# Kernel optimization log

Measured on AMD Instinct MI355X. Metric: run time of the kernel, lower is better.

The kernel has to match this reference:

```python
import jax, jax.numpy as jnp
import numpy as np
from jax import lax

B, T, D, H, K = 8, 1024, 1024, 16, 3
DK = D // H


def setup_inputs() -> dict:
    key = jax.random.key(0)
    ks = jax.random.split(key, 12)
    s = 0.02
    queries = jax.random.normal(ks[0], (B, T, D), dtype=jnp.float32)
    keys = jax.random.normal(ks[1], (B, T, D), dtype=jnp.float32)
    values = jax.random.normal(ks[2], (B, T, D), dtype=jnp.float32)
    # causal mask: True = masked (strict upper triangle)
    attn_mask = jnp.triu(jnp.ones((T, T), dtype=bool), k=1)
    # key padding mask: last 128 keys padded for every batch element
    src_key_padding_mask = jnp.broadcast_to(jnp.arange(T) >= T - 128, (B, T))
    conv_q_w = jax.random.normal(ks[3], (D, D, K), dtype=jnp.float32) * s  # (out, in, k)
    conv_q_b = jax.random.normal(ks[4], (D,), dtype=jnp.float32) * s
    conv_k_w = jax.random.normal(ks[5], (D, D, K), dtype=jnp.float32) * s
    conv_k_b = jax.random.normal(ks[6], (D,), dtype=jnp.float32) * s
    v_w = jax.random.normal(ks[7], (D, D), dtype=jnp.float32) * s   # torch Linear weight [out,in]
    v_b = jax.random.normal(ks[8], (D,), dtype=jnp.float32) * s
    out_w = jax.random.normal(ks[9], (D, D), dtype=jnp.float32) * s
    out_b = jax.random.normal(ks[10], (D,), dtype=jnp.float32) * s
    return {"queries": queries, "keys": keys, "values": values,
            "attn_mask": attn_mask, "src_key_padding_mask": src_key_padding_mask,
            "conv_q_w": conv_q_w, "conv_q_b": conv_q_b,
            "conv_k_w": conv_k_w, "conv_k_b": conv_k_b,
            "v_w": v_w, "v_b": v_b, "out_w": out_w, "out_b": out_b}


def _conv1d_same(x, w, b):
    # x: [B, T, D] -> conv over time with 'same' padding (pad_l=(K-1)//2, pad_r=K//2)
    pad_l, pad_r = (K - 1) // 2, K // 2
    xc = jnp.pad(x.transpose(0, 2, 1), ((0, 0), (0, 0), (pad_l, pad_r)))  # [B, D, T+K-1]
    y = lax.conv_general_dilated(xc, w, window_strides=(1,), padding='VALID',
                                 dimension_numbers=('NCH', 'OIH', 'NCH'))  # [B, D, T]
    return y.transpose(0, 2, 1) + b  # [B, T, D]


def _attention(queries, keys, values, attn_mask, key_padding_mask,
               conv_q_w, conv_q_b, conv_k_w, conv_k_b, v_w, v_b, out_w, out_b):
    q_out = _conv1d_same(queries, conv_q_w, conv_q_b)  # [B, Tq, D]
    k_out = _conv1d_same(keys, conv_k_w, conv_k_b)     # [B, Tk, D]
    v_out = values @ v_w.T + v_b                        # [B, Tk, D]

    Q = q_out.reshape(B, T, H, DK).transpose(0, 2, 1, 3)  # [B, H, Tq, dk]
    Kh = k_out.reshape(B, T, H, DK).transpose(0, 2, 1, 3)
    V = v_out.reshape(B, T, H, DK).transpose(0, 2, 1, 3)

    scores = jnp.einsum('bhqd,bhkd->bhqk', Q, Kh) / jnp.sqrt(jnp.float32(DK))
    neg = jnp.float32(-jnp.inf)
    scores = jnp.where(key_padding_mask[:, None, None, :], neg, scores)
    scores = jnp.where(attn_mask[None, None, :, :], neg, scores)
    attn_weights = jax.nn.softmax(scores, axis=-1)  # dropout is identity at eval
    attn_output = jnp.einsum('bhqk,bhkd->bhqd', attn_weights, V)
    attn_output = attn_output.transpose(0, 2, 1, 3).reshape(B, T, D)
    return attn_output @ out_w.T + out_b, attn_weights


def reference(queries, keys, values, attn_mask, src_key_padding_mask,
              conv_q_w, conv_q_b, conv_k_w, conv_k_b, v_w, v_b, out_w, out_b):
    return _attention(queries, keys, values, attn_mask, src_key_padding_mask,
                      conv_q_w, conv_q_b, conv_k_w, conv_k_b, v_w, v_b, out_w, out_b)
```

## Files before the change

### kernel.cpp

```cpp
#include <hip/hip_runtime.h>

typedef unsigned short u16;
typedef unsigned int   u32;
typedef __bf16 bf16x8 __attribute__((ext_vector_type(8)));
typedef float  f32x4  __attribute__((ext_vector_type(4)));
typedef const __attribute__((address_space(1))) u32* gas1_t;
typedef __attribute__((address_space(3))) u32*       las3_t;

#define DEV static __device__ __forceinline__
#define MFMA16(a, b, c) __builtin_amdgcn_mfma_f32_16x16x32_bf16((a), (b), (c), 0, 0, 0)

DEV u16 f2b(float f) {
  u32 u = __builtin_bit_cast(u32, f);
  return (u16)((u + 0x7fffu + ((u >> 16) & 1u)) >> 16);
}
DEV float b2f(u16 h) { return __builtin_bit_cast(float, (u32)h << 16); }

DEV void stage16(const void* g, void* l) {
  __builtin_amdgcn_global_load_lds((gas1_t)g, (las3_t)l, 16, 0, 0);
}

DEV int rfl(int x) { return __builtin_amdgcn_readfirstlane(x); }

extern "C" __global__ __launch_bounds__(256)
void k_prep(const float* __restrict__ s0, const float* __restrict__ s1,
            const float* __restrict__ s2, const float* __restrict__ s3,
            const float* __restrict__ s4, const float* __restrict__ wq,
            const float* __restrict__ wk, u16* __restrict__ dqkv,
            u16* __restrict__ dvw, u16* __restrict__ dow,
            u16* __restrict__ wtbase, u16* __restrict__ zbuf) {
  __shared__ float ls[3072];
  const int y = blockIdx.y, tid = threadIdx.x;
  if (y < 5) {
    const float* src = y == 0 ? s0 : y == 1 ? s1 : y == 2 ? s2 : y == 3 ? s3 : s4;
    u16* dst = y < 3 ? dqkv + (size_t)y * 8388608 : (y == 3 ? dvw : dow);
    const int n4 = y < 3 ? 2097152 : 262144;
    int i = blockIdx.x * 256 + tid;
    int st = gridDim.x * 256;
    for (; i < n4; i += st) {
      float4 v = ((const float4*)src)[i];
      ushort4 o;
      o.x = f2b(v.x); o.y = f2b(v.y); o.z = f2b(v.z); o.w = f2b(v.w);
      ((ushort4*)dst)[i] = o;
    }
  } else if (y < 7) {
    const int o = blockIdx.x, zz = y - 5;
    const float* src = (zz ? wk : wq) + (size_t)o * 3072;
#pragma unroll
    for (int s = 0; s < 3; ++s)
      ((float4*)ls)[s * 256 + tid] = ((const float4*)src)[s * 256 + tid];
    __syncthreads();
    u16* dst = wtbase + (size_t)zz * 3145728 + (size_t)o * 3072;
#pragma unroll
    for (int s = 0; s < 12; ++s) {
      int j = s * 256 + tid;
      int k = j >> 10, ii = j & 1023;
      dst[j] = f2b(ls[ii * 3 + k]);
    }
  } else {
    if (blockIdx.x == 0) zbuf[tid] = 0;
  }
}

template <int FUSED3, int OUTF32>
__global__ __launch_bounds__(256)
void k_gemm(const u16* __restrict__ Abase, const u16* __restrict__ Btbase,
            const float* __restrict__ b0, const float* __restrict__ b1,
            const float* __restrict__ b2, void* __restrict__ Cbase,
            u16* __restrict__ vT, const u16* __restrict__ zbuf) {
  __shared__ __align__(16) u16 smem[17408];
  const int z = FUSED3 ? blockIdx.z : 0;
  const bool conv = FUSED3 && (z < 2);
  const int K = conv ? 3072 : 1024;
  const u16* A = Abase + (size_t)z * 8388608;
  const u16* Bt = Btbase + (size_t)z * 3145728;
  const float* bias = z == 0 ? b0 : z == 1 ? b1 : b2;
  const int tid = threadIdx.x, lane = tid & 63, wave = tid >> 6;
  const int wm = wave >> 1, wn = wave & 1;
  const int l15 = lane & 15, gr = lane >> 4;
  const int r0 = blockIdx.y * 128, n0 = blockIdx.x * 128;
  const int srow = tid >> 3, scol = (tid & 7) * 8;
  u16* sA = smem;
  f32x4 acc[4][4] = {};

  if (conv) {
    u16* sB = smem + 8320;
    const int bb = r0 >> 10;
    const int tb = (r0 & 1023) - 1;
#pragma unroll 1
    for (int t = 0; t < 16; ++t) {
      const int c0 = t * 64;
#pragma unroll
      for (int s = 0; s < 5; ++s) {
        const int e = s * 256 + tid;
        if (e < 1040) {
          const int lr = e >> 3, ch = (e & 7) * 8;
          const int tt = tb + lr;
          const u16* g = ((u32)tt < 1024u)
              ? (A + (((size_t)((bb << 10) + tt)) << 10) + c0 + ch)
              : (zbuf + ch);
          stage16(g, (char*)smem + rfl((s * 256 + wave * 64) * 16));
        }
      }
#pragma unroll
      for (int s3 = 0; s3 < 3; ++s3) {
#pragma unroll
        for (int s = 0; s < 4; ++s) {
          const int row = s * 32 + srow;
          stage16(Bt + (size_t)(n0 + row) * 3072 + s3 * 1024 + c0 + scol,
                  (char*)smem + rfl(16640 + (s * 256 + wave * 64) * 16));
        }
        __syncthreads();
#pragma unroll
        for (int ks = 0; ks < 2; ++ks) {
          bf16x8 af[4], bfr[4];
          const int koff = ks * 32 + gr * 8;
#pragma unroll
          for (int f = 0; f < 4; ++f)
            af[f] = *(const bf16x8*)&sA[(wm * 64 + f * 16 + l15 + s3) * 64 + koff];
#pragma unroll
          for (int f = 0; f < 4; ++f)
            bfr[f] = *(const bf16x8*)&sB[(wn * 64 + f * 16 + l15) * 64 + koff];
#pragma unroll
          for (int i = 0; i < 4; ++i)
#pragma unroll
            for (int j = 0; j < 4; ++j)
              acc[i][j] = MFMA16(af[i], bfr[j], acc[i][j]);
        }
        __syncthreads();
      }
    }
  } else {
    u16* sB = smem + 8192;
    const int nt = K >> 6;
    for (int t = 0; t < nt; ++t) {
      const int k0 = t * 64;
#pragma unroll
      for (int s = 0; s < 4; ++s) {
        const int row = s * 32 + srow;
        stage16(A + (size_t)(r0 + row) * K + k0 + scol,
                (char*)smem + rfl((s * 256 + wave * 64) * 16));
        stage16(Bt + (size_t)(n0 + row) * K + k0 + scol,
                (char*)smem + rfl(16384 + (s * 256 + wave * 64) * 16));
      }
      __syncthreads();
#pragma unroll
      for (int ks = 0; ks < 2; ++ks) {
        bf16x8 af[4], bfr[4];
        const int koff = ks * 32 + gr * 8;
#pragma unroll
        for (int f = 0; f < 4; ++f)
          af[f] = *(const bf16x8*)&sA[(wm * 64 + f * 16 + l15) * 64 + koff];
#pragma unroll
        for (int f = 0; f < 4; ++f)
          bfr[f] = *(const bf16x8*)&sB[(wn * 64 + f * 16 + l15) * 64 + koff];
#pragma unroll
        for (int i = 0; i < 4; ++i)
#pragma unroll
          for (int j = 0; j < 4; ++j)
            acc[i][j] = MFMA16(af[i], bfr[j], acc[i][j]);
      }
      __syncthreads();
    }
  }

  if (FUSED3 && z == 2) {
    u16* tp = smem;
#pragma unroll
    for (int i = 0; i < 4; ++i)
#pragma unroll
      for (int j = 0; j < 4; ++j) {
        const int cl = wn * 64 + j * 16 + l15;
        const float bv = bias[n0 + cl];
        const int rl0 = wm * 64 + i * 16 + gr * 4;
        union { u16 h[4]; ushort4 v4; } tv;
#pragma unroll
        for (int r = 0; r < 4; ++r) tv.h[r] = f2b(acc[i][j][r] + bv);
        *(ushort4*)&tp[cl * 136 + rl0] = tv.v4;
      }
    __syncthreads();
    const int bb2 = r0 >> 10, tof = r0 & 1023;
    const int drb = tid >> 4, ch16 = (tid & 15) * 8;
#pragma unroll
    for (int g = 0; g < 8; ++g) {
      const int dr = g * 16 + drb;
      uint4 v4 = *(const uint4*)&tp[dr * 136 + ch16];
      *(uint4*)&vT[(((size_t)((bb2 << 10) + n0 + dr)) << 10) + tof + ch16] = v4;
    }
  } else {
    void* Cout = OUTF32 ? Cbase : (void*)((u16*)Cbase + (size_t)z * 8388608);
#pragma unroll
    for (int i = 0; i < 4; ++i)
#pragma unroll
      for (int j = 0; j < 4; ++j) {
        const int colg = n0 + wn * 64 + j * 16 + l15;
        const float bv = bias[colg];
#pragma unroll
        for (int r = 0; r < 4; ++r) {
          const int rowg = r0 + wm * 64 + i * 16 + gr * 4 + r;
          float v = acc[i][j][r] + bv;
          if (OUTF32) ((float*)Cout)[(size_t)rowg * 1024 + colg] = v;
          else        ((u16*)Cout)[(size_t)rowg * 1024 + colg] = f2b(v);
        }
      }
  }
}

__global__ __launch_bounds__(256)
void k_attn(const u16* __restrict__ Qg, const u16* __restrict__ Kg,
            const u16* __restrict__ Vtg, float* __restrict__ Wout,
            u16* __restrict__ Og) {
  __shared__ __align__(16) u16 sK[64 * 64];
  __shared__ __align__(16) u16 sV[64 * 64];
  __shared__ __align__(16) u16 sP[4][32 * 64];
  const int tid = threadIdx.x, lane = tid & 63, wave = tid >> 6;
  const int l15 = lane & 15, gr = lane >> 4;
  const int q0 = blockIdx.x * 128, h = blockIdx.y, b = blockIdx.z;
  const u16* Qh = Qg + ((size_t)b << 20) + h * 64;
  const u16* Kh = Kg + ((size_t)b << 20) + h * 64;
  const u16* Vh = Vtg + ((size_t)b << 20) + ((size_t)(h * 64) << 10);
  float* Wh = Wout + ((size_t)(b * 16 + h) << 20);
  const int qw0 = q0 + wave * 32;
  const int rmaxw = (qw0 + 31 < 895) ? (qw0 + 31) : 895;
  const int ktw = (rmaxw >> 6) + 1;
  const int rmaxg = (q0 + 127 < 895) ? (q0 + 127) : 895;
  const int ktmax = (rmaxg >> 6) + 1;

  bf16x8 qf[2][2];
#pragma unroll
  for (int i = 0; i < 2; ++i)
#pragma unroll
    for (int ks = 0; ks < 2; ++ks)
      qf[i][ks] = *(const bf16x8*)
          &Qh[(size_t)(qw0 + i * 16 + l15) * 1024 + ks * 32 + gr * 8];

  float l[2][4] = {};

  for (int kt = 0; kt < ktmax; ++kt) {
#pragma unroll
    for (int s = 0; s < 2; ++s) {
      int e = s * 256 + tid;
      int row = e >> 3, col = (e & 7) * 8;
      stage16(Kh + (size_t)(kt * 64 + row) * 1024 + col,
              (char*)sK + rfl((s * 256 + wave * 64) * 16));
    }
    __syncthreads();
    if (kt < ktw) {
      f32x4 sc[2][4] = {};
#pragma unroll
      for (int ks = 0; ks < 2; ++ks) {
        bf16x8 bfr[4];
        const int koff = ks * 32 + gr * 8;
#pragma unroll
        for (int f = 0; f < 4; ++f)
          bfr[f] = *(const bf16x8*)&sK[(f * 16 + l15) * 64 + koff];
#pragma unroll
        for (int i = 0; i < 2; ++i)
#pragma unroll
          for (int f = 0; f < 4; ++f) sc[i][f] = MFMA16(qf[i][ks], bfr[f], sc[i][f]);
      }
#pragma unroll
      for (int i = 0; i < 2; ++i)
#pragma unroll
        for (int r = 0; r < 4; ++r) {
          const int rowg = qw0 + i * 16 + gr * 4 + r;
          float ss = 0.f;
#pragma unroll
          for (int f = 0; f < 4; ++f) {
            const int colg = kt * 64 + f * 16 + l15;
            if (colg <= rowg && colg < 896) ss += __expf(sc[i][f][r] * 0.125f);
          }
#pragma unroll
          for (int d = 1; d < 16; d <<= 1) ss += __shfl_xor(ss, d, 16);
          l[i][r] += ss;
        }
    }
    __syncthreads();
  }

  float rl[2][4];
#pragma unroll
  for (int i = 0; i < 2; ++i)
#pragma unroll
    for (int r = 0; r < 4; ++r) rl[i][r] = 1.f / l[i][r];

  for (int r = 0; r < 32; ++r) {
    float* wrow = Wh + (size_t)(qw0 + r) * 1024;
    for (int c = ktw * 64 + lane * 4; c < 1024; c += 256)
      *(float4*)&wrow[c] = make_float4(0.f, 0.f, 0.f, 0.f);
  }

  f32x4 oa[2][4] = {};
  for (int kt = 0; kt < ktmax; ++kt) {
#pragma unroll
    for (int s = 0; s < 2; ++s) {
      int e = s * 256 + tid;
      int row = e >> 3, col = (e & 7) * 8;
      stage16(Kh + (size_t)(kt * 64 + row) * 1024 + col,
              (char*)sK + rfl((s * 256 + wave * 64) * 16));
      stage16(Vh + (size_t)row * 1024 + kt * 64 + col,
              (char*)sV + rfl((s * 256 + wave * 64) * 16));
    }
    __syncthreads();
    if (kt < ktw) {
      f32x4 sc[2][4] = {};
#pragma unroll
      for (int ks = 0; ks < 2; ++ks) {
        bf16x8 bfr[4];
        const int koff = ks * 32 + gr * 8;
#pragma unroll
        for (int f = 0; f < 4; ++f)
          bfr[f] = *(const bf16x8*)&sK[(f * 16 + l15) * 64 + koff];
#pragma unroll
        for (int i = 0; i < 2; ++i)
#pragma unroll
          for (int f = 0; f < 4; ++f) sc[i][f] = MFMA16(qf[i][ks], bfr[f], sc[i][f]);
      }
#pragma unroll
      for (int i = 0; i < 2; ++i)
#pragma unroll
        for (int r = 0; r < 4; ++r) {
          const int rowl = i * 16 + gr * 4 + r;
          const int rowg = qw0 + rowl;
#pragma unroll
          for (int f = 0; f < 4; ++f) {
            const int colt = f * 16 + l15;
            const int colg = kt * 64 + colt;
            float p = (colg <= rowg && colg < 896)
                          ? __expf(sc[i][f][r] * 0.125f) * rl[i][r] : 0.f;
            sP[wave][rowl * 64 + colt] = f2b(p);
          }
        }
      asm volatile("s_waitcnt lgkmcnt(0)" ::: "memory");
#pragma unroll
      for (int ks = 0; ks < 2; ++ks) {
        bf16x8 paf[2], vf[4];
        const int koff = ks * 32 + gr * 8;
        paf[0] = *(const bf16x8*)&sP[wave][l15 * 64 + koff];
        paf[1] = *(const bf16x8*)&sP[wave][(16 + l15) * 64 + koff];
#pragma unroll
        for (int f = 0; f < 4; ++f)
          vf[f] = *(const bf16x8*)&sV[(f * 16 + l15) * 64 + koff];
#pragma unroll
        for (int i = 0; i < 2; ++i)
#pragma unroll
          for (int f = 0; f < 4; ++f) oa[i][f] = MFMA16(paf[i], vf[f], oa[i][f]);
      }
#pragma unroll
      for (int rr = 0; rr < 8; ++rr) {
        const int rowl = rr * 4 + gr;
        const int c4 = l15 * 4;
        union { u16 h[4]; uint2 v2; } t;
        t.v2 = *(const uint2*)&sP[wave][rowl * 64 + c4];
        float4 o;
        o.x = b2f(t.h[0]); o.y = b2f(t.h[1]); o.z = b2f(t.h[2]); o.w = b2f(t.h[3]);
        *(float4*)&Wh[(size_t)(qw0 + rowl) * 1024 + kt * 64 + c4] = o;
      }
    }
    __syncthreads();
  }
#pragma unroll
  for (int i = 0; i < 2; ++i)
#pragma unroll
    for (int f = 0; f < 4; ++f)
#pragma unroll
      for (int r = 0; r < 4; ++r) {
        const int rowg = qw0 + i * 16 + gr * 4 + r;
        const int dd = f * 16 + l15;
        Og[((size_t)b * 1024 + rowg) * 1024 + h * 64 + dd] = f2b(oa[i][f][r]);
      }
}

extern "C" void kernel_launch(void* const* d_in, const int* in_sizes, int n_in,
                              void* d_out, int out_size, void* d_ws, size_t ws_size,
                              hipStream_t stream) {
  const float* queries  = (const float*)d_in[0];
  const float* keys     = (const float*)d_in[1];
  const float* values   = (const float*)d_in[2];
  const float* conv_q_w = (const float*)d_in[5];
  const float* conv_q_b = (const float*)d_in[6];
  const float* conv_k_w = (const float*)d_in[7];
  const float* conv_k_b = (const float*)d_in[8];
  const float* v_w      = (const float*)d_in[9];
  const float* v_b      = (const float*)d_in[10];
  const float* out_w    = (const float*)d_in[11];
  const float* out_b    = (const float*)d_in[12];

  float* out0 = (float*)d_out;
  float* outW = out0 + (size_t)8 * 1024 * 1024;

  char* W = (char*)d_ws;
  u16* qkv_bf = (u16*)(W + (size_t)0);
  u16* wt     = (u16*)(W + (size_t)50331648);
  u16* ow_t   = (u16*)(W + (size_t)65011712);
  u16* q_out  = (u16*)(W + (size_t)67108864);
  u16* zbuf   = (u16*)(W + (size_t)117440512);
  u16* vw_t   = wt + (size_t)2 * 3145728;
  u16* k_out  = q_out + (size_t)8388608;
  u16* v_outT = q_out + (size_t)2 * 8388608;
  u16* a_out  = qkv_bf + 8388608;

  dim3 blk(256);
  k_prep<<<dim3(1024, 8), blk, 0, stream>>>(queries, keys, values, v_w, out_w,
                                            conv_q_w, conv_k_w, qkv_bf, vw_t,
                                            ow_t, wt, zbuf);

  k_gemm<1, 0><<<dim3(8, 64, 3), blk, 0, stream>>>(
      qkv_bf, wt, conv_q_b, conv_k_b, v_b, (void*)q_out, v_outT, zbuf);
  k_attn<<<dim3(8, 16, 8), blk, 0, stream>>>(q_out, k_out, v_outT, outW, a_out);
  k_gemm<0, 1><<<dim3(8, 64, 1), blk, 0, stream>>>(
      a_out, ow_t, out_b, out_b, out_b, (void*)out0, v_outT, zbuf);
}
```

Before: 445.3 us.

## Split conv GEMMs into dedicated 512-thread kernel with 128x256 tiles

The Q/K convolution GEMMs move out of the fused 3-way k_gemm into a new k_conv512 kernel. It uses 512 threads and 128x256 output tiles, so each staged A tile (with its halo rows) is reused across twice as many output columns. The V projection now runs as a separate k_gemm launch selected by a z offset. This cuts A-tile reloads for the conv path, in exchange for an extra launch, higher LDS use per block, and uncoalesced scalar bf16 stores in the epilogue.

```diff
diff --git a/kernel.cpp b/kernel.cpp
--- a/kernel.cpp
+++ b/kernel.cpp
@@ -62,16 +62,95 @@
   }
 }
 
+extern "C" __global__ __launch_bounds__(512)
+void k_conv512(const u16* __restrict__ Abase, const u16* __restrict__ Btbase,
+               const float* __restrict__ b0, const float* __restrict__ b1,
+               u16* __restrict__ Cbase, const u16* __restrict__ zbuf) {
+  __shared__ __align__(16) u16 smem[24704];
+  const int bid = blockIdx.x;
+  const int xz = bid & 7;
+  const int z = xz >> 2;
+  const int n0 = (xz & 3) * 256;
+  const int r0 = (bid >> 3) * 128;
+  const u16* A = Abase + (size_t)z * 8388608;
+  const u16* Bt = Btbase + (size_t)z * 3145728;
+  const float* bias = z ? b1 : b0;
+  const int tid = threadIdx.x, lane = tid & 63, wave = tid >> 6;
+  const int wm = wave >> 2, wn = wave & 3;
+  const int l15 = lane & 15, gr = lane >> 4;
+  const int srow = tid >> 3, scol = (tid & 7) * 8;
+  u16* sA = smem;
+  u16* sB = smem + 8320;
+  f32x4 acc[4][4] = {};
+  const int bb = r0 >> 10;
+  const int tb = (r0 & 1023) - 1;
+#pragma unroll 1
+  for (int t = 0; t < 16; ++t) {
+    const int c0 = t * 64;
+#pragma unroll
+    for (int s = 0; s < 3; ++s) {
+      const int e = s * 512 + tid;
+      if (e < 1040) {
+        const int lr = e >> 3, ch = (e & 7) * 8;
+        const int tt = tb + lr;
+        const u16* g = ((u32)tt < 1024u)
+            ? (A + (((size_t)((bb << 10) + tt)) << 10) + c0 + ch)
+            : (zbuf + ch);
+        stage16(g, (char*)smem + rfl((s * 512 + wave * 64) * 16));
+      }
+    }
+#pragma unroll
+    for (int s3 = 0; s3 < 3; ++s3) {
+#pragma unroll
+      for (int s = 0; s < 4; ++s) {
+        const int row = s * 64 + srow;
+        stage16(Bt + (size_t)(n0 + row) * 3072 + s3 * 1024 + c0 + scol,
+                (char*)smem + rfl(16640 + (s * 512 + wave * 64) * 16));
+      }
+      __syncthreads();
+#pragma unroll
+      for (int ks = 0; ks < 2; ++ks) {
+        bf16x8 af[4], bfr[4];
+        const int koff = ks * 32 + gr * 8;
+#pragma unroll
+        for (int f = 0; f < 4; ++f)
+          af[f] = *(const bf16x8*)&sA[(wm * 64 + f * 16 + l15 + s3) * 64 + koff];
+#pragma unroll
+        for (int f = 0; f < 4; ++f)
+          bfr[f] = *(const bf16x8*)&sB[(wn * 64 + f * 16 + l15) * 64 + koff];
+#pragma unroll
+        for (int i = 0; i < 4; ++i)
+#pragma unroll
+          for (int j = 0; j < 4; ++j)
+            acc[i][j] = MFMA16(af[i], bfr[j], acc[i][j]);
+      }
+      __syncthreads();
+    }
+  }
+  u16* Cout = Cbase + (size_t)z * 8388608;
+#pragma unroll
+  for (int i = 0; i < 4; ++i)
+#pragma unroll
+    for (int j = 0; j < 4; ++j) {
+      const int colg = n0 + wn * 64 + j * 16 + l15;
+      const float bv = bias[colg];
+#pragma unroll
+      for (int r = 0; r < 4; ++r) {
+        const int rowg = r0 + wm * 64 + i * 16 + gr * 4 + r;
+        Cout[(size_t)rowg * 1024 + colg] = f2b(acc[i][j][r] + bv);
+      }
+    }
+}
+
 template <int FUSED3, int OUTF32>
 __global__ __launch_bounds__(256)
 void k_gemm(const u16* __restrict__ Abase, const u16* __restrict__ Btbase,
             const float* __restrict__ b0, const float* __restrict__ b1,
             const float* __restrict__ b2, void* __restrict__ Cbase,
-            u16* __restrict__ vT, const u16* __restrict__ zbuf) {
+            u16* __restrict__ vT, const u16* __restrict__ zbuf, int zoff) {
   __shared__ __align__(16) u16 smem[17408];
-  const int z = FUSED3 ? blockIdx.z : 0;
-  const bool conv = FUSED3 && (z < 2);
-  const int K = conv ? 3072 : 1024;
+  const int z = FUSED3 ? ((int)blockIdx.z + zoff) : 0;
+  const int K = 1024;
   const u16* A = Abase + (size_t)z * 8388608;
   const u16* Bt = Btbase + (size_t)z * 3145728;
   const float* bias = z == 0 ? b0 : z == 1 ? b1 : b2;
@@ -81,87 +160,38 @@
   const int r0 = blockIdx.y * 128, n0 = blockIdx.x * 128;
   const int srow = tid >> 3, scol = (tid & 7) * 8;
   u16* sA = smem;
+  u16* sB = smem + 8192;
   f32x4 acc[4][4] = {};
 
-  if (conv) {
-    u16* sB = smem + 8320;
-    const int bb = r0 >> 10;
-    const int tb = (r0 & 1023) - 1;
-#pragma unroll 1
-    for (int t = 0; t < 16; ++t) {
-      const int c0 = t * 64;
-#pragma unroll
-      for (int s = 0; s < 5; ++s) {
-        const int e = s * 256 + tid;
-        if (e < 1040) {
-          const int lr = e >> 3, ch = (e & 7) * 8;
-          const int tt = tb + lr;
-          const u16* g = ((u32)tt < 1024u)
-              ? (A + (((size_t)((bb << 10) + tt)) << 10) + c0 + ch)
-              : (zbuf + ch);
-          stage16(g, (char*)smem + rfl((s * 256 + wave * 64) * 16));
-        }
-      }
-#pragma unroll
-      for (int s3 = 0; s3 < 3; ++s3) {
-#pragma unroll
-        for (int s = 0; s < 4; ++s) {
-          const int row = s * 32 + srow;
-          stage16(Bt + (size_t)(n0 + row) * 3072 + s3 * 1024 + c0 + scol,
-                  (char*)smem + rfl(16640 + (s * 256 + wave * 64) * 16));
-        }
-        __syncthreads();
-#pragma unroll
-        for (int ks = 0; ks < 2; ++ks) {
-          bf16x8 af[4], bfr[4];
-          const int koff = ks * 32 + gr * 8;
-#pragma unroll
-          for (int f = 0; f < 4; ++f)
-            af[f] = *(const bf16x8*)&sA[(wm * 64 + f * 16 + l15 + s3) * 64 + koff];
-#pragma unroll
-          for (int f = 0; f < 4; ++f)
-            bfr[f] = *(const bf16x8*)&sB[(wn * 64 + f * 16 + l15) * 64 + koff];
-#pragma unroll
-          for (int i = 0; i < 4; ++i)
-#pragma unroll
-            for (int j = 0; j < 4; ++j)
-              acc[i][j] = MFMA16(af[i], bfr[j], acc[i][j]);
-        }
-        __syncthreads();
-      }
-    }
-  } else {
-    u16* sB = smem + 8192;
-    const int nt = K >> 6;
-    for (int t = 0; t < nt; ++t) {
-      const int k0 = t * 64;
-#pragma unroll
-      for (int s = 0; s < 4; ++s) {
-        const int row = s * 32 + srow;
-        stage16(A + (size_t)(r0 + row) * K + k0 + scol,
-                (char*)smem + rfl((s * 256 + wave * 64) * 16));
-        stage16(Bt + (size_t)(n0 + row) * K + k0 + scol,
-                (char*)smem + rfl(16384 + (s * 256 + wave * 64) * 16));
-      }
-      __syncthreads();
-#pragma unroll
-      for (int ks = 0; ks < 2; ++ks) {
-        bf16x8 af[4], bfr[4];
-        const int koff = ks * 32 + gr * 8;
-#pragma unroll
-        for (int f = 0; f < 4; ++f)
-          af[f] = *(const bf16x8*)&sA[(wm * 64 + f * 16 + l15) * 64 + koff];
-#pragma unroll
-        for (int f = 0; f < 4; ++f)
-          bfr[f] = *(const bf16x8*)&sB[(wn * 64 + f * 16 + l15) * 64 + koff];
-#pragma unroll
-        for (int i = 0; i < 4; ++i)
-#pragma unroll
-          for (int j = 0; j < 4; ++j)
-            acc[i][j] = MFMA16(af[i], bfr[j], acc[i][j]);
-      }
-      __syncthreads();
-    }
+  const int nt = K >> 6;
+  for (int t = 0; t < nt; ++t) {
+    const int k0 = t * 64;
+#pragma unroll
+    for (int s = 0; s < 4; ++s) {
+      const int row = s * 32 + srow;
+      stage16(A + (size_t)(r0 + row) * K + k0 + scol,
+              (char*)smem + rfl((s * 256 + wave * 64) * 16));
+      stage16(Bt + (size_t)(n0 + row) * K + k0 + scol,
+              (char*)smem + rfl(16384 + (s * 256 + wave * 64) * 16));
+    }
+    __syncthreads();
+#pragma unroll
+    for (int ks = 0; ks < 2; ++ks) {
+      bf16x8 af[4], bfr[4];
+      const int koff = ks * 32 + gr * 8;
+#pragma unroll
+      for (int f = 0; f < 4; ++f)
+        af[f] = *(const bf16x8*)&sA[(wm * 64 + f * 16 + l15) * 64 + koff];
+#pragma unroll
+      for (int f = 0; f < 4; ++f)
+        bfr[f] = *(const bf16x8*)&sB[(wn * 64 + f * 16 + l15) * 64 + koff];
+#pragma unroll
+      for (int i = 0; i < 4; ++i)
+#pragma unroll
+        for (int j = 0; j < 4; ++j)
+          acc[i][j] = MFMA16(af[i], bfr[j], acc[i][j]);
+    }
+    __syncthreads();
   }
 
   if (FUSED3 && z == 2) {
@@ -331,7 +361,7 @@
             sP[wave][rowl * 64 + colt] = f2b(p);
           }
         }
-      asm volatile("s_waitcnt lgkmcnt(0)" ::: "memory");
+    asm volatile("s_waitcnt lgkmcnt(0)" ::: "memory");
 #pragma unroll
       for (int ks = 0; ks < 2; ++ks) {
         bf16x8 paf[2], vf[4];
@@ -405,9 +435,11 @@
                                             conv_q_w, conv_k_w, qkv_bf, vw_t,
                                             ow_t, wt, zbuf);
 
-  k_gemm<1, 0><<<dim3(8, 64, 3), blk, 0, stream>>>(
-      qkv_bf, wt, conv_q_b, conv_k_b, v_b, (void*)q_out, v_outT, zbuf);
+  k_conv512<<<dim3(512), dim3(512), 0, stream>>>(
+      qkv_bf, wt, conv_q_b, conv_k_b, q_out, zbuf);
+  k_gemm<1, 0><<<dim3(8, 64, 1), blk, 0, stream>>>(
+      qkv_bf, wt, conv_q_b, conv_k_b, v_b, (void*)q_out, v_outT, zbuf, 2);
   k_attn<<<dim3(8, 16, 8), blk, 0, stream>>>(q_out, k_out, v_outT, outW, a_out);
   k_gemm<0, 1><<<dim3(8, 64, 1), blk, 0, stream>>>(
-      a_out, ow_t, out_b, out_b, out_b, (void*)out0, v_outT, zbuf);
-}
+      a_out, ow_t, out_b, out_b, out_b, (void*)out0, v_outT, zbuf, 0);
+}
```

Measured after the change: 486.9 us. +9.3%, slower.
